# Optimization experiments

Hardware: AMD Instinct MI355X
Metric: run time of the kernel (lower is better)

## Reference

```python
import jax, jax.numpy as jnp
import numpy as np

N_VOCAB = 50257
N_EMBED = 300
N_HIDDEN = 256
N_OUTPUT = 1
BATCH = 256
SEQ_LEN = 512


def setup_inputs() -> dict:
    key = jax.random.key(0)
    k1, k2, k3, k4, k5, k6 = jax.random.split(key, 6)
    input_words = jax.random.randint(k1, (BATCH, SEQ_LEN), 0, N_VOCAB, dtype=jnp.int64 if jax.config.jax_enable_x64 else jnp.int32)
    emb_table = jax.random.normal(k2, (N_VOCAB, N_EMBED), dtype=jnp.float32)
    Wi = jax.random.normal(k3, (N_EMBED, N_HIDDEN), dtype=jnp.float32)
    Wh = jax.random.normal(k4, (N_HIDDEN, N_HIDDEN), dtype=jnp.float32)
    # nn.Linear default init: U(-1/sqrt(in), 1/sqrt(in))
    bound = 1.0 / np.sqrt(N_HIDDEN)
    fc_w = jax.random.uniform(k5, (N_HIDDEN, N_OUTPUT), minval=-bound, maxval=bound, dtype=jnp.float32)
    fc_b = jax.random.uniform(k6, (N_OUTPUT,), minval=-bound, maxval=bound, dtype=jnp.float32)
    return {"input_words": input_words, "emb_table": emb_table, "Wi": Wi, "Wh": Wh, "fc_w": fc_w, "fc_b": fc_b}


def reference(input_words, emb_table, Wi, Wh, fc_w, fc_b):
    # [B, S, E] -> [S, B, E] (module permutes to time-major)
    embedded = emb_table[input_words].transpose(1, 0, 2)
    h0 = jnp.zeros((input_words.shape[0], Wh.shape[0]), dtype=embedded.dtype)

    def step(h, x_t):
        # recurrence: h = sigmoid(x_t @ Wi + h @ Wh)
        h_new = jax.nn.sigmoid(x_t @ Wi + h @ Wh)
        return h_new, None

    hidden, _ = jax.lax.scan(step, h0, embedded)
    sig = jax.nn.sigmoid(hidden @ fc_w + fc_b)
    return (sig, hidden)
```

## Files before the change

kernel.cpp:

```cpp
#include <hip/hip_runtime.h>

#define S_LEN 512
#define BATCH 256
#define EMB   300
#define HID   256
#define VOCAB 50257
#define NPROD 786
#define NLOG2E -1.44269504089f

#define EW_BYTES 25731584ull

typedef __attribute__((ext_vector_type(8))) _Float16 f16x8;
typedef __attribute__((ext_vector_type(4))) _Float16 f16x4;
typedef __attribute__((ext_vector_type(2))) __fp16   fp16v2;
typedef __attribute__((ext_vector_type(4))) float    f32x4;

__device__ __forceinline__ void block_sync_lds() {
    asm volatile("" ::: "memory");
    __builtin_amdgcn_s_waitcnt(0xC07F);
    __builtin_amdgcn_s_barrier();
    asm volatile("" ::: "memory");
}

__device__ __forceinline__ float sigmoid_scaled(float xs) {
    float e = __builtin_amdgcn_exp2f(xs);
    return __builtin_amdgcn_rcpf(1.0f + e);
}

__global__ __launch_bounds__(256, 1)
void k_embwi(const float* __restrict__ emb, const float* __restrict__ Wi,
             _Float16* __restrict__ EW) {
    const int tid  = threadIdx.x;
    const int wv   = tid >> 6;
    const int lane = tid & 63;
    const int ln   = lane & 15;
    const int q    = lane >> 4;
    const int m0   = blockIdx.x * 64;

    f16x8 bfrag[10][4];
#pragma unroll
    for (int kc = 0; kc < 10; kc++) {
#pragma unroll
        for (int nt = 0; nt < 4; nt++) {
            const int n = wv * 64 + nt * 16 + ln;
            f16x8 u;
#pragma unroll
            for (int j = 0; j < 8; j++) {
                const int k = kc * 32 + q * 8 + j;
                u[j] = (k < EMB) ? (_Float16)(Wi[k * HID + n] * NLOG2E) : (_Float16)0.f;
            }
            bfrag[kc][nt] = u;
        }
    }

    const float* arow[4];
#pragma unroll
    for (int mt = 0; mt < 4; mt++) {
        int row = m0 + mt * 16 + ln; if (row >= VOCAB) row = VOCAB - 1;
        arow[mt] = emb + (long)row * EMB + q * 8;
    }

    auto load_af = [&](int kc, int mt) -> f16x8 {
        const float* p = arow[mt] + kc * 32;
        f16x8 v;
        if (kc < 9 || q == 0) {
            f32x4 a = *(const f32x4*)p;
            f32x4 b = *(const f32x4*)(p + 4);
#pragma unroll
            for (int r = 0; r < 4; r++) { v[r] = (_Float16)a[r]; v[4 + r] = (_Float16)b[r]; }
        } else if (q == 1) {
            f32x4 a = *(const f32x4*)p;
#pragma unroll
            for (int r = 0; r < 4; r++) { v[r] = (_Float16)a[r]; v[4 + r] = (_Float16)0.f; }
        } else {
#pragma unroll
            for (int r = 0; r < 8; r++) v[r] = (_Float16)0.f;
        }
        return v;
    };

    f32x4 acc[4][4];
#pragma unroll
    for (int mt = 0; mt < 4; mt++)
#pragma unroll
        for (int nt = 0; nt < 4; nt++)
            acc[mt][nt] = f32x4{0.f, 0.f, 0.f, 0.f};

    f16x8 af[4], afn[4];
#pragma unroll
    for (int mt = 0; mt < 4; mt++) af[mt] = load_af(0, mt);

#pragma unroll
    for (int kc = 0; kc < 10; kc++) {
        if (kc < 9) {
#pragma unroll
            for (int mt = 0; mt < 4; mt++) afn[mt] = load_af(kc + 1, mt);
        }
#pragma unroll
        for (int mt = 0; mt < 4; mt++)
#pragma unroll
            for (int nt = 0; nt < 4; nt++)
                acc[mt][nt] = __builtin_amdgcn_mfma_f32_16x16x32_f16(
                    af[mt], bfrag[kc][nt], acc[mt][nt], 0, 0, 0);
#pragma unroll
        for (int mt = 0; mt < 4; mt++) af[mt] = afn[mt];
    }

#pragma unroll
    for (int mt = 0; mt < 4; mt++)
#pragma unroll
        for (int nt = 0; nt < 4; nt++) {
            const int col = wv * 64 + nt * 16 + ln;
#pragma unroll
            for (int r = 0; r < 4; r++) {
                const int mm = m0 + mt * 16 + q * 4 + r;
                if (mm < VOCAB) EW[(long)mm * HID + col] = (_Float16)acc[mt][nt][r];
            }
        }
}

__global__ __launch_bounds__(256)
void k_expand(const int* __restrict__ words, const _Float16* __restrict__ EW,
              _Float16* __restrict__ As) {
    const int g  = blockIdx.x * 256 + threadIdx.x;
    const int e0 = g << 3;
    const int t  = e0 >> 16;
    const int b  = (e0 >> 8) & 255;
    const int j0 = e0 & 255;
    const _Float16* src = EW + ((long)words[b * S_LEN + t] << 8) + j0;
    *(f16x8*)(As + e0) = *(const f16x8*)src;
}

#define HSTR 264
#define HB8  (8 * HSTR)

__global__ __launch_bounds__(512, 2)
void k_recur(const float* __restrict__ Wh, const _Float16* __restrict__ As,
             const float* __restrict__ fcw, const float* __restrict__ fcb,
             float* __restrict__ out) {
    __shared__ __attribute__((aligned(16))) _Float16 hbuf[2 * HB8];
    __shared__ float red[512];

    const int tid  = threadIdx.x;
    const int wv   = tid >> 6;
    const int lane = tid & 63;
    const int ln   = lane & 15;
    const int lnn  = ln & 7;
    const int q    = lane >> 4;
    const int b0   = blockIdx.x * 8;

    f16x8 whf[8][2];
#pragma unroll
    for (int kc = 0; kc < 8; kc++) {
#pragma unroll
        for (int mt = 0; mt < 2; mt++) {
            const int j = wv * 32 + mt * 16 + ln;
            f16x8 u;
#pragma unroll
            for (int jj = 0; jj < 8; jj++)
                u[jj] = (_Float16)(Wh[(kc * 32 + q * 8 + jj) * HID + j] * NLOG2E);
            whf[kc][mt] = u;
        }
    }

    for (int i = tid; i < 2 * HB8; i += 512) hbuf[i] = (_Float16)0.f;
    __syncthreads();

    const int jbase = wv * 32 + q * 4;
    const _Float16* abase = As + (long)(b0 + lnn) * HID + jbase;
    f16x4 abuf0[2], abuf1[2];
#pragma unroll
    for (int mt = 0; mt < 2; mt++) abuf0[mt] = *(const f16x4*)(abase + 0L * 65536 + mt * 16);
#pragma unroll
    for (int mt = 0; mt < 2; mt++) abuf1[mt] = *(const f16x4*)(abase + 1L * 65536 + mt * 16);

#define STEP(T, ABUF)                                                                   \
    {                                                                                   \
        const int tt = (T);                                                             \
        const _Float16* hr = hbuf + ((tt & 1) ? HB8 : 0);                               \
        _Float16*       hw = hbuf + ((tt & 1) ? 0 : HB8);                               \
        f16x8 hf[8];                                                                    \
        _Pragma("unroll")                                                               \
        for (int kc = 0; kc < 8; kc++)                                                  \
            hf[kc] = *(const f16x8*)(hr + lnn * HSTR + kc * 32 + q * 8);                \
        f32x4 acc_a[2], acc_b[2];                                                       \
        _Pragma("unroll")                                                               \
        for (int mt = 0; mt < 2; mt++) {               \
            f16x4 av = ABUF[mt];                                                        \
            acc_a[mt] = f32x4{(float)av[0], (float)av[1], (float)av[2], (float)av[3]};  \
            acc_b[mt] = f32x4{0.f, 0.f, 0.f, 0.f};                                      \
        }                                                                               \
        const long t2 = (tt + 2 > 511) ? 511 : (tt + 2);                                \
        const _Float16* rp = abase + t2 * 65536;                                        \
        _Pragma("unroll")                                                               \
        for (int mt = 0; mt < 2; mt++) ABUF[mt] = *(const f16x4*)(rp + mt * 16);        \
        _Pragma("unroll")                                                               \
        for (int r = 0; r < 4; r++) {                            \
            _Pragma("unroll")                                                           \
            for (int mt = 0; mt < 2; mt++)                                              \
                acc_a[mt] = __builtin_amdgcn_mfma_f32_16x16x32_f16(                     \
                    whf[r][mt], hf[r], acc_a[mt], 0, 0, 0);                             \
            _Pragma("unroll")                                                           \
            for (int mt = 0; mt < 2; mt++)                                              \
                acc_b[mt] = __builtin_amdgcn_mfma_f32_16x16x32_f16(                     \
                    whf[r + 4][mt], hf[r + 4], acc_b[mt], 0, 0, 0);                     \
        }                                                                               \
        _Pragma("unroll")                                                               \
        for (int mt = 0; mt < 2; mt++) {                                                \
            f32x4 s = acc_a[mt] + acc_b[mt];                                            \
            float r0 = sigmoid_scaled(s[0]), r1 = sigmoid_scaled(s[1]);                 \
            float r2 = sigmoid_scaled(s[2]), r3 = sigmoid_scaled(s[3]);                 \
            union { fp16v2 h2[2]; f16x4 v4; } hp;                                       \
            hp.h2[0] = __builtin_amdgcn_cvt_pkrtz(r0, r1);                              \
            hp.h2[1] = __builtin_amdgcn_cvt_pkrtz(r2, r3);                              \
            if (ln < 8)                                                                 \
                *(f16x4*)(hw + ln * HSTR + wv * 32 + mt * 16 + q * 4) = hp.v4;          \
        }                                                                               \
        block_sync_lds();                                                               \
    }

    for (int t = 0; t < S_LEN; t += 2) {
        STEP(t, abuf0);
        STEP(t + 1, abuf1);
    }
#undef STEP

    const _Float16* hf0 = hbuf;

    {
        const int row = tid >> 6, j0 = (tid & 63) * 4;
        float* dst = out + 256 + (long)(b0 + row) * HID + j0;
        f32x4 w;
#pragma unroll
        for (int r = 0; r < 4; r++) w[r] = (float)hf0[row * HSTR + j0 + r];
        *(f32x4*)dst = w;
    }

    {
        const int row = tid >> 6, part = tid & 63;
        float s = 0.f;
#pragma unroll
        for (int jj = 0; jj < 4; jj++) {
            const int j = part * 4 + jj;
            s += (float)hf0[row * HSTR + j] * fcw[j];
        }
        red[row * 64 + part] = s;
    }
    __syncthreads();
    if (tid < 8) {
        float s = fcb[0];
#pragma unroll
        for (int p = 0; p < 64; p++) s += red[tid * 64 + p];
        s *= NLOG2E;
        out[b0 + tid] = sigmoid_scaled(s);
    }
}

extern "C" void kernel_launch(void* const* d_in, const int* in_sizes, int n_in,
                              void* d_out, int out_size, void* d_ws, size_t ws_size,
                              hipStream_t stream) {
    const int*   words = (const int*)d_in[0];
    const float* emb   = (const float*)d_in[1];
    const float* Wi    = (const float*)d_in[2];
    const float* Wh    = (const float*)d_in[3];
    const float* fcw   = (const float*)d_in[4];
    const float* fcb   = (const float*)d_in[5];
    _Float16* EW   = (_Float16*)d_ws;
    _Float16* As   = (_Float16*)((char*)d_ws + EW_BYTES);
    float*    outp = (float*)d_out;

    hipLaunchKernelGGL(k_embwi,  dim3(NPROD), dim3(256), 0, stream, emb, Wi, EW);
    hipLaunchKernelGGL(k_expand, dim3(16384), dim3(256), 0, stream, words, EW, As);
    hipLaunchKernelGGL(k_recur,  dim3(BATCH / 8), dim3(512), 0, stream,
                       Wh, As, fcw, fcb, outp);
}
```

Before: 454.6 us.

## Fuse gather-expand into recurrence kernel with producer/consumer atomic counters

Replaces the separate expand kernel with a fused launch where 32 consumer blocks run the recurrence and 512 producer blocks each gather one timestep of projected embeddings into As. They coordinate through per-8-timestep atomic counters that consumers spin on, so the recurrence can start before all gathering completes. Intent is to overlap the expand memory traffic with the serial recurrence and remove a kernel boundary. The scheme relies on the consumer blocks being resident alongside producers and adds spin-wait and fence overhead.

```diff
diff --git a/kernel.cpp b/kernel.cpp
--- a/kernel.cpp
+++ b/kernel.cpp
@@ -8,7 +8,8 @@
 #define NPROD 786
 #define NLOG2E -1.44269504089f
 
-#define EW_BYTES 25731584ull
+#define EW_BYTES  25731584ull
+#define AS_BYTES  67108864ull
 
 typedef __attribute__((ext_vector_type(8))) _Float16 f16x8;
 typedef __attribute__((ext_vector_type(4))) _Float16 f16x4;
@@ -29,8 +30,10 @@
 
 __global__ __launch_bounds__(256, 1)
 void k_embwi(const float* __restrict__ emb, const float* __restrict__ Wi,
-             _Float16* __restrict__ EW) {
+             _Float16* __restrict__ EW, unsigned int* __restrict__ cnt) {
     const int tid  = threadIdx.x;
+    if (blockIdx.x == 0 && tid < 64) cnt[tid] = 0u;
+
     const int wv   = tid >> 6;
     const int lane = tid & 63;
     const int ln   = lane & 15;
@@ -119,25 +122,38 @@
         }
 }
 
-__global__ __launch_bounds__(256)
-void k_expand(const int* __restrict__ words, const _Float16* __restrict__ EW,
-              _Float16* __restrict__ As) {
-    const int g  = blockIdx.x * 256 + threadIdx.x;
-    const int e0 = g << 3;
-    const int t  = e0 >> 16;
-    const int b  = (e0 >> 8) & 255;
-    const int j0 = e0 & 255;
-    const _Float16* src = EW + ((long)words[b * S_LEN + t] << 8) + j0;
-    *(f16x8*)(As + e0) = *(const f16x8*)src;
-}
-
 #define HSTR 264
 #define HB8  (8 * HSTR)
 
-__global__ __launch_bounds__(512, 2)
-void k_recur(const float* __restrict__ Wh, const _Float16* __restrict__ As,
-             const float* __restrict__ fcw, const float* __restrict__ fcb,
-             float* __restrict__ out) {
+__device__ void producer_body(int t, const int* __restrict__ words,
+                              const _Float16* __restrict__ EW,
+                              _Float16* __restrict__ As,
+                              unsigned int* __restrict__ cnt) {
+    const int tid = threadIdx.x;
+    _Float16* dst = As + (long)t * 65536;
+    for (int i = tid; i < 8192; i += 512) {
+        const int e  = i << 3;
+        const int b  = e >> 8;
+        const int j0 = e & 255;
+        const _Float16* src = EW + ((long)words[b * S_LEN + t] << 8) + j0;
+        *(f16x8*)(dst + e) = *(const f16x8*)src;
+    }
+    __syncthreads();
+    if (tid == 0) {
+        __threadfence();
+        __hip_atomic_fetch_add(&cnt[t >> 3], 1u,
+                               __ATOMIC_RELEASE, __HIP_MEMORY_SCOPE_AGENT);
+    }
+}
+
+__device__ __forceinline__ void wait_group(unsigned int* cnt, int g) {
+    while (__hip_atomic_load(&cnt[g], __ATOMIC_ACQUIRE, __HIP_MEMORY_SCOPE_AGENT) < 8u)
+        __builtin_amdgcn_s_sleep(2);
+}
+
+__device__ void consumer_body(const float* __restrict__ Wh, const _Float16* __restrict__ As,
+                              const float* __restrict__ fcw, const float* __restrict__ fcb,
+                              float* __restrict__ out, unsigned int* __restrict__ cnt) {
     __shared__ __attribute__((aligned(16))) _Float16 hbuf[2 * HB8];
     __shared__ float red[512];
 
@@ -166,6 +182,8 @@
     for (int i = tid; i < 2 * HB8; i += 512) hbuf[i] = (_Float16)0.f;
     __syncthreads();
 
+    wait_group(cnt, 0);
+
     const int jbase = wv * 32 + q * 4;
     const _Float16* abase = As + (long)(b0 + lnn) * HID + jbase;
     f16x4 abuf0[2], abuf1[2];
@@ -185,7 +203,7 @@
             hf[kc] = *(const f16x8*)(hr + lnn * HSTR + kc * 32 + q * 8);                \
         f32x4 acc_a[2], acc_b[2];                                                       \
         _Pragma("unroll")                                                               \
-        for (int mt = 0; mt < 2; mt++) {               \
+        for (int mt = 0; mt < 2; mt++) {                                                \
             f16x4 av = ABUF[mt];                                                        \
             acc_a[mt] = f32x4{(float)av[0], (float)av[1], (float)av[2], (float)av[3]};  \
             acc_b[mt] = f32x4{0.f, 0.f, 0.f, 0.f};                                      \
@@ -195,7 +213,7 @@
         _Pragma("unroll")                                                               \
         for (int mt = 0; mt < 2; mt++) ABUF[mt] = *(const f16x4*)(rp + mt * 16);        \
         _Pragma("unroll")                                                               \
-        for (int r = 0; r < 4; r++) {                            \
+        for (int r = 0; r < 4; r++) {                                                   \
             _Pragma("unroll")                                                           \
             for (int mt = 0; mt < 2; mt++)                                              \
                 acc_a[mt] = __builtin_amdgcn_mfma_f32_16x16x32_f16(                     \
@@ -219,9 +237,14 @@
         block_sync_lds();                                                               \
     }
 
-    for (int t = 0; t < S_LEN; t += 2) {
-        STEP(t, abuf0);
-        STEP(t + 1, abuf1);
+    for (int g = 0; g < 64; g++) {
+        wait_group(cnt, (g + 1 > 63) ? 63 : g + 1);
+        const int t0 = g * 8;
+#pragma unroll
+        for (int u = 0; u < 8; u += 2) {
+            STEP(t0 + u,     abuf0);
+            STEP(t0 + u + 1, abuf1);
+        }
     }
 #undef STEP
 
@@ -254,6 +277,15 @@
         s *= NLOG2E;
         out[b0 + tid] = sigmoid_scaled(s);
     }
+}
+
+__global__ __launch_bounds__(512, 2)
+void k_fused(const int* __restrict__ words, const _Float16* __restrict__ EW,
+             const float* __restrict__ Wh, _Float16* __restrict__ As,
+             const float* __restrict__ fcw, const float* __restrict__ fcb,
+             unsigned int* __restrict__ cnt, float* __restrict__ out) {
+    if (blockIdx.x < 32) consumer_body(Wh, As, fcw, fcb, out, cnt);
+    else                 producer_body(blockIdx.x - 32, words, EW, As, cnt);
 }
 
 extern "C" void kernel_launch(void* const* d_in, const int* in_sizes, int n_in,
@@ -265,12 +297,12 @@
     const float* Wh    = (const float*)d_in[3];
     const float* fcw   = (const float*)d_in[4];
     const float* fcb   = (const float*)d_in[5];
-    _Float16* EW   = (_Float16*)d_ws;
-    _Float16* As   = (_Float16*)((char*)d_ws + EW_BYTES);
-    float*    outp = (float*)d_out;
-
-    hipLaunchKernelGGL(k_embwi,  dim3(NPROD), dim3(256), 0, stream, emb, Wi, EW);
-    hipLaunchKernelGGL(k_expand, dim3(16384), dim3(256), 0, stream, words, EW, As);
-    hipLaunchKernelGGL(k_recur,  dim3(BATCH / 8), dim3(512), 0, stream,
-                       Wh, As, fcw, fcb, outp);
-}
+    _Float16*     EW   = (_Float16*)d_ws;
+    _Float16*     As   = (_Float16*)((char*)d_ws + EW_BYTES);
+    unsigned int* cnt  = (unsigned int*)((char*)d_ws + EW_BYTES + AS_BYTES);
+    float*        outp = (float*)d_out;
+
+    hipLaunchKernelGGL(k_embwi, dim3(NPROD), dim3(256), 0, stream, emb, Wi, EW, cnt);
+    hipLaunchKernelGGL(k_fused, dim3(32 + S_LEN), dim3(512), 0, stream,
+                       words, EW, Wh, As, fcw, fcb, cnt, outp);
+}
```

After: 515.1 us. +13.3%, slower.
